# Kernel optimization log

Measured on AMD Instinct MI355X. Metric: run time of the kernel, lower is better.

Reference implementation:

```python
import jax, jax.numpy as jnp
import numpy as np

B, S, D = 2, 2048, 2048
H = 16
HD = D // H
FF = 8192
EPS = 1e-5


def _layer_norm(x, g, b):
    mu = jnp.mean(x, axis=-1, keepdims=True)
    var = jnp.mean(jnp.square(x - mu), axis=-1, keepdims=True)
    return (x - mu) * jax.lax.rsqrt(var + EPS) * g + b


def setup_inputs() -> dict:
    key = jax.random.key(0)
    ks = jax.random.split(key, 8)
    s = 0.02
    return {
        "x": jax.random.normal(ks[0], (B, S, D), dtype=jnp.float32),
        "ln1_g": jnp.ones((D,), jnp.float32),
        "ln1_b": jnp.zeros((D,), jnp.float32),
        "qkv_w": jax.random.normal(ks[1], (D, 3 * D), dtype=jnp.float32) * s,
        "qkv_b": jnp.zeros((3 * D,), jnp.float32),
        "out_w": jax.random.normal(ks[2], (D, D), dtype=jnp.float32) * s,
        "out_b": jnp.zeros((D,), jnp.float32),
        "ln2_g": jnp.ones((D,), jnp.float32),
        "ln2_b": jnp.zeros((D,), jnp.float32),
        "w1": jax.random.normal(ks[3], (D, FF), dtype=jnp.float32) * s,
        "b1": jnp.zeros((FF,), jnp.float32),
        "w2": jax.random.normal(ks[4], (FF, D), dtype=jnp.float32) * s,
        "b2": jnp.zeros((D,), jnp.float32),
    }


def reference(x, ln1_g, ln1_b, qkv_w, qkv_b, out_w, out_b, ln2_g, ln2_b, w1, b1, w2, b2):
    # --- attention sub-block (pre-norm) ---
    residual = x
    h = _layer_norm(x, ln1_g, ln1_b)
    qkv = h @ qkv_w + qkv_b                      # [B,S,3D]
    q, k, v = jnp.split(qkv, 3, axis=-1)
    # [B,S,D] -> [B,H,S,HD]
    q = q.reshape(B, S, H, HD).transpose(0, 2, 1, 3)
    k = k.reshape(B, S, H, HD).transpose(0, 2, 1, 3)
    v = v.reshape(B, S, H, HD).transpose(0, 2, 1, 3)
    scores = jnp.einsum("bhqd,bhkd->bhqk", q, k)  # [B,H,S,S]
    causal = jnp.triu(jnp.ones((S, S), dtype=bool), k=1)
    scores = jnp.where(causal[None, None], -jnp.inf, scores)
    attn = jax.nn.softmax(scores / np.sqrt(HD).astype(np.float32), axis=-1)
    av = jnp.einsum("bhqk,bhkd->bhqd", attn, v)   # [B,H,S,HD]
    av = av.transpose(0, 2, 1, 3).reshape(B, S, D)
    x = residual + (av @ out_w + out_b)
    # --- FFN sub-block (pre-norm) ---
    residual = x
    h = _layer_norm(x, ln2_g, ln2_b)
    h = jax.nn.gelu(h @ w1 + b1, approximate=False)
    x = residual + (h @ w2 + b2)
    return x
```

## Files before the change

### kernel.cpp

```cpp
#include <hip/hip_runtime.h>
#include <hip/hip_bf16.h>

#define B_  2
#define S_  2048
#define D_  2048
#define H_  16
#define HD_ 128
#define FF_ 8192

typedef __bf16 bf16x8 __attribute__((ext_vector_type(8)));
typedef float  f32x4  __attribute__((ext_vector_type(4)));
typedef unsigned short u16;
typedef u16 u16x8 __attribute__((ext_vector_type(8)));

__device__ __forceinline__ u16 f2bf(float f) {
    union { float f; unsigned u; } c; c.f = f;
    unsigned u = c.u;
    u += 0x7fffu + ((u >> 16) & 1u);
    return (u16)(u >> 16);
}

__device__ __forceinline__ void gld16(void* lds, const void* g) {
    __builtin_amdgcn_global_load_lds(
        (const __attribute__((address_space(1))) unsigned int*)g,
        (__attribute__((address_space(3))) unsigned int*)lds,
        16, 0, 0);
}

__global__ __launch_bounds__(256)
void ln_kernel(const float* __restrict__ x, const float* __restrict__ g,
               const float* __restrict__ bb, u16* __restrict__ out)
{
    int row = blockIdx.x, tid = threadIdx.x;
    const float4* xr = (const float4*)(x + (size_t)row * D_);
    float4 a = xr[tid], c = xr[tid + 256];
    float s  = a.x + a.y + a.z + a.w + c.x + c.y + c.z + c.w;
    float s2 = a.x*a.x + a.y*a.y + a.z*a.z + a.w*a.w
             + c.x*c.x + c.y*c.y + c.z*c.z + c.w*c.w;
    #pragma unroll
    for (int off = 32; off > 0; off >>= 1) {
        s  += __shfl_down(s,  off, 64);
        s2 += __shfl_down(s2, off, 64);
    }
    __shared__ float red[16];
    __shared__ float mr[2];
    int wid = tid >> 6, lane = tid & 63;
    if (lane == 0) { red[wid] = s; red[8 + wid] = s2; }
    __syncthreads();
    if (tid == 0) {
        float ts = red[0] + red[1] + red[2] + red[3];
        float t2 = red[8] + red[9] + red[10] + red[11];
        float mu = ts * (1.0f / D_);
        float var = t2 * (1.0f / D_) - mu * mu;
        mr[0] = mu; mr[1] = rsqrtf(var + 1e-5f);
    }
    __syncthreads();
    float mu = mr[0], rstd = mr[1];
    const float4* gg = (const float4*)g;
    const float4* bv = (const float4*)bb;
    float4 g0 = gg[tid], g1 = gg[tid + 256];
    float4 b0 = bv[tid], b1 = bv[tid + 256];
    u16* orow = out + (size_t)row * D_;
    ushort4 o0, o1;
    o0.x = f2bf((a.x - mu) * rstd * g0.x + b0.x);
    o0.y = f2bf((a.y - mu) * rstd * g0.y + b0.y);
    o0.z = f2bf((a.z - mu) * rstd * g0.z + b0.z);
    o0.w = f2bf((a.w - mu) * rstd * g0.w + b0.w);
    o1.x = f2bf((c.x - mu) * rstd * g1.x + b1.x);
    o1.y = f2bf((c.y - mu) * rstd * g1.y + b1.y);
    o1.z = f2bf((c.z - mu) * rstd * g1.z + b1.z);
    o1.w = f2bf((c.w - mu) * rstd * g1.w + b1.w);
    *(ushort4*)&orow[tid * 4]         = o0;
    *(ushort4*)&orow[(tid + 256) * 4] = o1;
}

__global__ __launch_bounds__(256)
void tcvt_kernel(const float* __restrict__ W, u16* __restrict__ WT, int K, int N)
{
    __shared__ float t[32][33];
    int n0 = blockIdx.x << 5, k0 = blockIdx.y << 5;
    int tx = threadIdx.x & 31, ty = threadIdx.x >> 5;
    #pragma unroll
    for (int i = 0; i < 32; i += 8)
        t[ty + i][tx] = W[(size_t)(k0 + ty + i) * N + n0 + tx];
    __syncthreads();
    #pragma unroll
    for (int i = 0; i < 32; i += 8)
        WT[(size_t)(n0 + ty + i) * K + k0 + tx] = f2bf(t[tx][ty + i]);
}

template<int EPI>
__global__ __launch_bounds__(256)
void gemm_kernel(const u16* __restrict__ A, const u16* __restrict__ BT,
                 const float* __restrict__ bias, const float* __restrict__ res,
                 void* __restrict__ outv, int M, int N, int K)
{
    __shared__ u16 ldsA[128 * 64];
    __shared__ u16 ldsB[128 * 64];
    int tid = threadIdx.x;
    int wid = tid >> 6, lane = tid & 63;
    int wm = wid >> 1, wn = wid & 1;
    int quad = lane >> 4, l16 = lane & 15;

    int tiles_m = M >> 7;
    int bandsz = tiles_m << 4;
    int lin = blockIdx.x;
    int band = lin / bandsz, rr = lin % bandsz;
    int m0 = (rr >> 4) << 7;
    int n0 = ((band << 4) + (rr & 15)) << 7;

    f32x4 acc[4][4] = {};

    int r8 = lane >> 3, c8 = lane & 7;
    int gc = (c8 ^ (r8 & 7)) << 3;
    const u16* pA = A  + (size_t)(m0 + wid * 32 + r8) * K + gc;
    const u16* pB = BT + (size_t)(n0 + wid * 32 + r8) * K + gc;
    u16* lA = ldsA + wid * 32 * 64;
    u16* lB = ldsB + wid * 32 * 64;
    int sw = l16 & 7;

    for (int k0 = 0; k0 < K; k0 += 64) {
        #pragma unroll
        for (int j = 0; j < 4; j++) {
            gld16(lA + j * 512, pA + (size_t)j * 8 * K + k0);
            gld16(lB + j * 512, pB + (size_t)j * 8 * K + k0);
        }
        __syncthreads();
        #pragma unroll
        for (int kk = 0; kk < 2; kk++) {
            bf16x8 af[4], bf[4];
            int co0 = ((kk * 4 + 0) ^ sw) << 3;
            int co1 = ((kk * 4 + 1) ^ sw) << 3;
            int co2 = ((kk * 4 + 2) ^ sw) << 3;
            int co3 = ((kk * 4 + 3) ^ sw) << 3;
            int co = quad == 0 ? co0 : quad == 1 ? co1 : quad == 2 ? co2 : co3;
            #pragma unroll
            for (int t = 0; t < 4; t++) {
                af[t] = *(const bf16x8*)&ldsA[(wm * 64 + t * 16 + l16) * 64 + co];
                bf[t] = *(const bf16x8*)&ldsB[(wn * 64 + t * 16 + l16) * 64 + co];
            }
            #pragma unroll
            for (int i = 0; i < 4; i++)
                #pragma unroll
                for (int j = 0; j < 4; j++)
                    acc[i][j] = __builtin_amdgcn_mfma_f32_16x16x32_bf16(af[i], bf[j], acc[i][j], 0, 0, 0);
        }
        __syncthreads();
    }

    u16*   outb = (u16*)outv;
    float* outf = (float*)outv;
    int colb = n0 + wn * 64, rowb = m0 + wm * 64;
    #pragma unroll
    for (int j = 0; j < 4; j++) {
        int col = colb + j * 16 + l16;
        float bv = bias[col];
        #pragma unroll
        for (int i = 0; i < 4; i++) {
            int row0 = rowb + i * 16 + (quad << 2);
            #pragma unroll
            for (int r = 0; r < 4; r++) {
                float v = acc[i][j][r] + bv;
                size_t idx = (size_t)(row0 + r) * N + col;
                if (EPI == 2) {
                    outf[idx] = v + res[idx];
                } else {
                    if (EPI == 1) v = 0.5f * v * (1.0f + erff(v * 0.70710678118654752f));
                    outb[idx] = f2bf(v);
                }
            }
        }
    }
}

__global__ __launch_bounds__(256, 2)
void attn_kernel(const u16* __restrict__ qkv, u16* __restrict__ av)
{
    __shared__ u16 ldsK[4][64][32];
    __shared__ unsigned ldsVT[128][36];
    __shared__ u16 ldsP[4][32][72];
    int tid = threadIdx.x, wid = tid >> 6, lane = tid & 63;
    int quad = lane >> 4, l16 = lane & 15;
    int bh = blockIdx.y, b = bh >> 4, h = bh & 15;
    int qx = gridDim.x - 1 - blockIdx.x;
    int q0 = qx << 7;
    const u16* base = qkv + (size_t)b * S_ * (3 * D_);

    bf16x8 aq[2][4];
    #pragma unroll
    for (int set = 0; set < 2; set++) {
        int qrow = q0 + set * 64 + wid * 16 + l16;
        const u16* qp = base + (size_t)qrow * (3 * D_) + h * HD_;
        #pragma unroll
        for (int kk = 0; kk < 4; kk++)
            aq[set][kk] = *(const bf16x8*)(qp + kk * 32 + quad * 8);
    }

    float m_i[2][4], l_i[2][4];
    f32x4 oacc[2][8] = {};
    #pragma unroll
    for (int s = 0; s < 2; s++)
        #pragma unroll
        for (int r = 0; r < 4; r++) { m_i[s][r] = -1e30f; l_i[s][r] = 0.f; }

    const float scale = 0.088388347648318447f;
    int ntile = 2 * qx + 2;
    for (int jt = 0; jt < ntile; jt++) {
        int j0 = jt << 6;
        #pragma unroll
        for (int j = 0; j < 4; j++) {
            int c = wid * 4 + j;
            int kk = c >> 2, kb = c & 3;
            int key = (kb << 4) + (lane >> 2);
            const u16* g = base + (size_t)(j0 + key) * (3 * D_) + D_ + h * HD_
                         + kk * 32 + ((lane & 3) << 3);
            gld16((u16*)ldsK + c * 512, g);
        }
        {
            int kp = lane & 31, dhalf = lane >> 5;
            #pragma unroll
            for (int p = 0; p < 2; p++) {
                int doff = wid * 32 + p * 16 + dhalf * 8;
                const u16* g0 = base + (size_t)(j0 + 2 * kp) * (3 * D_)
                              + 2 * D_ + h * HD_ + doff;
                u16x8 v0 = *(const u16x8*)g0;
                u16x8 v1 = *(const u16x8*)(g0 + 3 * D_);
                #pragma unroll
                for (int k = 0; k < 8; k++)
                    ldsVT[doff + k][kp] = (unsigned)v0[k] | ((unsigned)v1[k] << 16);
            }
        }
        __syncthreads();
        f32x4 sacc[2][4] = {};
        #pragma unroll
        for (int kk = 0; kk < 4; kk++)
            #pragma unroll
            for (int n = 0; n < 4; n++) {
                bf16x8 bfr = *(const bf16x8*)&ldsK[kk][(n << 4) + l16][quad << 3];
                sacc[0][n] = __builtin_amdgcn_mfma_f32_16x16x32_bf16(aq[0][kk], bfr, sacc[0][n], 0, 0, 0);
                sacc[1][n] = __builtin_amdgcn_mfma_f32_16x16x32_bf16(aq[1][kk], bfr, sacc[1][n], 0, 0, 0);
            }
        #pragma unroll
        for (int set = 0; set < 2; set++) {
            float rowmax[4] = {-1e30f, -1e30f, -1e30f, -1e30f};
            #pragma unroll
            for (int n = 0; n < 4; n++) {
                int key = j0 + (n << 4) + l16;
                #pragma unroll
                for (int r = 0; r < 4; r++) {
                    float xv = sacc[set][n][r] * scale;
                    int qr = q0 + set * 64 + wid * 16 + (quad << 2) + r;
                    if (key > qr) xv = -1e30f;
                    sacc[set][n][r] = xv;
                    rowmax[r] = fmaxf(rowmax[r], xv);
                }
            }
            #pragma unroll
            for (int off = 1; off < 16; off <<= 1)
                #pragma unroll
                for (int r = 0; r < 4; r++)
                    rowmax[r] = fmaxf(rowmax[r], __shfl_xor(rowmax[r], off, 64));
            float alpha[4], rsum[4];
            #pragma unroll
            for (int r = 0; r < 4; r++) {
                float mn = fmaxf(m_i[set][r], rowmax[r]);
                alpha[r] = __expf(m_i[set][r] - mn);
                m_i[set][r] = mn;
                rsum[r] = 0.f;
            }
            #pragma unroll
            for (int n = 0; n < 4; n++)
                #pragma unroll
                for (int r = 0; r < 4; r++) {
                    float p = __expf(sacc[set][n][r] - m_i[set][r]);
                    rsum[r] += p;
                    ldsP[wid][set * 16 + (quad << 2) + r][(n << 4) + l16] = f2bf(p);
                }
            #pragma unroll
            for (int off = 1; off < 16; off <<= 1)
                #pragma unroll
                for (int r = 0; r < 4; r++)
                    rsum[r] += __shfl_xor(rsum[r], off, 64);
            #pragma unroll
            for (int r = 0; r < 4; r++)
                l_i[set][r] = l_i[set][r] * alpha[r] + rsum[r];
            #pragma unroll
            for (int n = 0; n < 8; n++)
                #pragma unroll
                for (int r = 0; r < 4; r++)
                    oacc[set][n][r] *= alpha[r];
        }
        #pragma unroll
        for (int ks = 0; ks < 2; ks++) {
            bf16x8 pa0 = *(const bf16x8*)&ldsP[wid][l16]     [(ks << 5) + (quad << 3)];
            bf16x8 pa1 = *(const bf16x8*)&ldsP[wid][16 + l16][(ks << 5) + (quad << 3)];
            #pragma unroll
            for (int n = 0; n < 8; n++) {
                bf16x8 vb = *(const bf16x8*)&ldsVT[(n << 4) + l16][(ks << 4) + (quad << 2)];
                oacc[0][n] = __builtin_amdgcn_mfma_f32_16x16x32_bf16(pa0, vb, oacc[0][n], 0, 0, 0);
                oacc[1][n] = __builtin_amdgcn_mfma_f32_16x16x32_bf16(pa1, vb, oacc[1][n], 0, 0, 0);
            }
        }
        __syncthreads();
    }
    #pragma unroll
    for (int set = 0; set < 2; set++)
        #pragma unroll
        for (int r = 0; r < 4; r++) {
            float inv = 1.0f / l_i[set][r];
            int qr = q0 + set * 64 + wid * 16 + (quad << 2) + r;
            u16* op = av + (size_t)(b * S_ + qr) * D_ + h * HD_;
            #pragma unroll
            for (int n = 0; n < 8; n++)
                op[(n << 4) + l16] = f2bf(oacc[set][n][r] * inv);
        }
}

extern "C" void kernel_launch(void* const* d_in, const int* in_sizes, int n_in,
                              void* d_out, int out_size, void* d_ws, size_t ws_size,
                              hipStream_t stream)
{
    const float* x     = (const float*)d_in[0];
    const float* ln1_g = (const float*)d_in[1];
    const float* ln1_b = (const float*)d_in[2];
    const float* qkv_w = (const float*)d_in[3];
    const float* qkv_b = (const float*)d_in[4];
    const float* out_w = (const float*)d_in[5];
    const float* out_b = (const float*)d_in[6];
    const float* ln2_g = (const float*)d_in[7];
    const float* ln2_b = (const float*)d_in[8];
    const float* w1    = (const float*)d_in[9];
    const float* b1    = (const float*)d_in[10];
    const float* w2    = (const float*)d_in[11];
    const float* b2    = (const float*)d_in[12];
    float* out = (float*)d_out;

    char* ws  = (char*)d_ws;
    u16* wT   = (u16*)ws;
    u16* hbuf = (u16*)(ws + (32u << 20));
    u16* big  = (u16*)(ws + (48u << 20));
    u16* qkvb = big;
    u16* ffb  = big;

    dim3 blk(256);

    ln_kernel<<<dim3(B_ * S_), blk, 0, stream>>>(x, ln1_g, ln1_b, hbuf);
    tcvt_kernel<<<dim3(6144 / 32, 2048 / 32), blk, 0, stream>>>(qkv_w, wT, 2048, 6144);
    gemm_kernel<0><<<dim3((6144 / 128) * (4096 / 128)), blk, 0, stream>>>(
        hbuf, wT, qkv_b, nullptr, (void*)qkvb, 4096, 6144, 2048);
    attn_kernel<<<dim3(S_ / 128, B_ * H_), blk, 0, stream>>>(qkvb, hbuf);
    tcvt_kernel<<<dim3(2048 / 32, 2048 / 32), blk, 0, stream>>>(out_w, wT, 2048, 2048);
    gemm_kernel<2><<<dim3((2048 / 128) * (4096 / 128)), blk, 0, stream>>>(
        hbuf, wT, out_b, x, (void*)out, 4096, 2048, 2048);
    ln_kernel<<<dim3(B_ * S_), blk, 0, stream>>>(out, ln2_g, ln2_b, hbuf);
    tcvt_kernel<<<dim3(8192 / 32, 2048 / 32), blk, 0, stream>>>(w1, wT, 2048, 8192);
    gemm_kernel<1><<<dim3((8192 / 128) * (4096 / 128)), blk, 0, stream>>>(
        hbuf, wT, b1, nullptr, (void*)ffb, 4096, 8192, 2048);
    tcvt_kernel<<<dim3(2048 / 32, 8192 / 32), blk, 0, stream>>>(w2, wT, 8192, 2048);
    gemm_kernel<2><<<dim3((2048 / 128) * (4096 / 128)), blk, 0, stream>>>(
        ffb, wT, b2, out, (void*)out, 4096, 2048, 8192);
}
```

Measured before the change: 951.7 us.

## Load GEMM MFMA fragments directly from global memory with register double buffering

```diff
diff --git a/kernel.cpp b/kernel.cpp
--- a/kernel.cpp
+++ b/kernel.cpp
@@ -95,8 +95,6 @@
                  const float* __restrict__ bias, const float* __restrict__ res,
                  void* __restrict__ outv, int M, int N, int K)
 {
-    __shared__ u16 ldsA[128 * 64];
-    __shared__ u16 ldsB[128 * 64];
     int tid = threadIdx.x;
     int wid = tid >> 6, lane = tid & 63;
     int wm = wid >> 1, wn = wid & 1;
@@ -111,42 +109,59 @@
 
     f32x4 acc[4][4] = {};
 
-    int r8 = lane >> 3, c8 = lane & 7;
-    int gc = (c8 ^ (r8 & 7)) << 3;
-    const u16* pA = A  + (size_t)(m0 + wid * 32 + r8) * K + gc;
-    const u16* pB = BT + (size_t)(n0 + wid * 32 + r8) * K + gc;
-    u16* lA = ldsA + wid * 32 * 64;
-    u16* lB = ldsB + wid * 32 * 64;
-    int sw = l16 & 7;
-
-    for (int k0 = 0; k0 < K; k0 += 64) {
-        #pragma unroll
-        for (int j = 0; j < 4; j++) {
-            gld16(lA + j * 512, pA + (size_t)j * 8 * K + k0);
-            gld16(lB + j * 512, pB + (size_t)j * 8 * K + k0);
-        }
-        __syncthreads();
-        #pragma unroll
-        for (int kk = 0; kk < 2; kk++) {
-            bf16x8 af[4], bf[4];
-            int co0 = ((kk * 4 + 0) ^ sw) << 3;
-            int co1 = ((kk * 4 + 1) ^ sw) << 3;
-            int co2 = ((kk * 4 + 2) ^ sw) << 3;
-            int co3 = ((kk * 4 + 3) ^ sw) << 3;
-            int co = quad == 0 ? co0 : quad == 1 ? co1 : quad == 2 ? co2 : co3;
-            #pragma unroll
-            for (int t = 0; t < 4; t++) {
-                af[t] = *(const bf16x8*)&ldsA[(wm * 64 + t * 16 + l16) * 64 + co];
-                bf[t] = *(const bf16x8*)&ldsB[(wn * 64 + t * 16 + l16) * 64 + co];
-            }
-            #pragma unroll
-            for (int i = 0; i < 4; i++)
-                #pragma unroll
-                for (int j = 0; j < 4; j++)
-                    acc[i][j] = __builtin_amdgcn_mfma_f32_16x16x32_bf16(af[i], bf[j], acc[i][j], 0, 0, 0);
-        }
-        __syncthreads();
-    }
+    const u16* pa[4];
+    const u16* pb[4];
+    #pragma unroll
+    for (int t = 0; t < 4; t++) {
+        pa[t] = A  + (size_t)(m0 + wm * 64 + t * 16 + l16) * K + quad * 8;
+        pb[t] = BT + (size_t)(n0 + wn * 64 + t * 16 + l16) * K + quad * 8;
+    }
+
+    bf16x8 f0a[4], f0b[4], f1a[4], f1b[4];
+    #pragma unroll
+    for (int t = 0; t < 4; t++) {
+        f0a[t] = *(const bf16x8*)(pa[t]);
+        f0b[t] = *(const bf16x8*)(pb[t]);
+    }
+
+    int k0 = 0;
+    for (; k0 < K - 64; k0 += 64) {
+        #pragma unroll
+        for (int t = 0; t < 4; t++) {
+            f1a[t] = *(const bf16x8*)(pa[t] + k0 + 32);
+            f1b[t] = *(const bf16x8*)(pb[t] + k0 + 32);
+        }
+        #pragma unroll
+        for (int i = 0; i < 4; i++)
+            #pragma unroll
+            for (int j = 0; j < 4; j++)
+                acc[i][j] = __builtin_amdgcn_mfma_f32_16x16x32_bf16(f0a[i], f0b[j], acc[i][j], 0, 0, 0);
+        #pragma unroll
+        for (int t = 0; t < 4; t++) {
+            f0a[t] = *(const bf16x8*)(pa[t] + k0 + 64);
+            f0b[t] = *(const bf16x8*)(pb[t] + k0 + 64);
+        }
+        #pragma unroll
+        for (int i = 0; i < 4; i++)
+            #pragma unroll
+            for (int j = 0; j < 4; j++)
+                acc[i][j] = __builtin_amdgcn_mfma_f32_16x16x32_bf16(f1a[i], f1b[j], acc[i][j], 0, 0, 0);
+    }
+    #pragma unroll
+    for (int t = 0; t < 4; t++) {
+        f1a[t] = *(const bf16x8*)(pa[t] + k0 + 32);
+        f1b[t] = *(const bf16x8*)(pb[t] + k0 + 32);
+    }
+    #pragma unroll
+    for (int i = 0; i < 4; i++)
+        #pragma unroll
+        for (int j = 0; j < 4; j++)
+            acc[i][j] = __builtin_amdgcn_mfma_f32_16x16x32_bf16(f0a[i], f0b[j], acc[i][j], 0, 0, 0);
+    #pragma unroll
+    for (int i = 0; i < 4; i++)
+        #pragma unroll
+        for (int j = 0; j < 4; j++)
+            acc[i][j] = __builtin_amdgcn_mfma_f32_16x16x32_bf16(f1a[i], f1b[j], acc[i][j], 0, 0, 0);
 
     u16*   outb = (u16*)outv;
     float* outf = (float*)outv;
```

After: 1.839 ms. 93.2% more time.
